# Kernel tuning notes

Hardware: AMD Instinct MI355X
Metric: run time of the kernel (lower is better)

## Reference

```python
import jax, jax.numpy as jnp
import numpy as np

PROPOSAL_NUM = 6          # max_output_size in tf.image.non_max_suppression
IOU_THRESHOLD = 0.25      # boxes with IoU > 0.25 vs a selected box are suppressed
CANVAS = 448.0            # NTS-Net input image size


def setup_inputs() -> dict:
    key = jax.random.key(0)
    k1, k2, k3 = jax.random.split(key, 3)
    B, N = 512, 65536
    rpn_score = jax.random.normal(k1, (B, N), dtype=jnp.float32)
    # anchors in [y1, x1, y2, x2] format with y2>y1, x2>x1 (as tf.image.non_max_suppression expects)
    yx1 = jax.random.uniform(k2, (N, 2), dtype=jnp.float32, minval=0.0, maxval=CANVAS)
    hw = jax.random.uniform(k3, (N, 2), dtype=jnp.float32, minval=16.0, maxval=200.0)
    anchors = jnp.concatenate([yx1, yx1 + hw], axis=-1)  # [N, 4]
    return {"rpn_score": rpn_score, "anchors": anchors}


def _batched_nms(rpn_score, anchors, k, iou_thr):
    """Greedy NMS, vectorized over the batch. Matches tf.image.non_max_suppression
    semantics with score_threshold=-inf: repeatedly pick the highest-scoring active
    box, then deactivate all boxes whose IoU with it exceeds iou_thr."""
    B, N = rpn_score.shape
    y1, x1, y2, x2 = anchors[:, 0], anchors[:, 1], anchors[:, 2], anchors[:, 3]
    areas = (y2 - y1) * (x2 - x1)            # [N]
    batch_ix = jnp.arange(B)

    def step(active, _):
        # active: [B, N] bool mask of boxes still eligible
        s = jnp.where(active, rpn_score, -jnp.inf)
        idx = jnp.argmax(s, axis=-1)          # [B] index of best remaining box
        sel = anchors[idx]                    # [B, 4]
        # IoU of selected box against all anchors -> [B, N]
        iy1 = jnp.maximum(sel[:, 0:1], y1[None, :])
        ix1 = jnp.maximum(sel[:, 1:2], x1[None, :])
        iy2 = jnp.minimum(sel[:, 2:3], y2[None, :])
        ix2 = jnp.minimum(sel[:, 3:4], x2[None, :])
        inter = jnp.maximum(iy2 - iy1, 0.0) * jnp.maximum(ix2 - ix1, 0.0)
        union = areas[idx][:, None] + areas[None, :] - inter
        iou = inter / union
        active = active & (iou <= iou_thr)
        active = active.at[batch_ix, idx].set(False)  # selected box itself removed
        return active, idx

    active0 = jnp.ones((B, N), dtype=bool)
    _, idxs = jax.lax.scan(step, active0, None, length=k)  # idxs: [k, B]
    return jnp.transpose(idxs).astype(jnp.int32)            # [B, k]


def reference(rpn_score, anchors):
    return _batched_nms(rpn_score, anchors, PROPOSAL_NUM, IOU_THRESHOLD)
```

## Files before the change

### kernel.cpp

```cpp
#include <hip/hip_runtime.h>


constexpr int N_BOX = 65536;
constexpr int KSEL  = 6;
constexpr int NT    = 1024;
constexpr int EPT   = N_BOX / NT;
constexpr float THR = 0.25f;

__device__ __forceinline__ unsigned long long umax64(unsigned long long a,
                                                     unsigned long long b) {
    return a > b ? a : b;
}

__global__ __launch_bounds__(NT) void nms_kernel(
    const float* __restrict__ score,
    const float* __restrict__ anchors,
    int* __restrict__ out)
{
    const int b    = blockIdx.x;
    const int tid  = threadIdx.x;
    const int base = tid * EPT;

    unsigned long long t0 = 0, t1 = 0, t2 = 0, t3 = 0;
    {
        const float4* s4 = reinterpret_cast<const float4*>(score + (size_t)b * N_BOX + base);
        const unsigned nb = ~(unsigned)base;
        #pragma unroll
        for (int q = 0; q < EPT / 4; ++q) {
            float4 v = s4[q];
            #pragma unroll
            for (int e = 0; e < 4; ++e) {
                unsigned fb = __float_as_uint(e == 0 ? v.x : e == 1 ? v.y : e == 2 ? v.z : v.w);
                unsigned m  = fb ^ (unsigned)(((int)fb >> 31) | 0x80000000);
                unsigned long long k =
                    ((unsigned long long)m << 32) | (unsigned)(nb - (4 * q + e));
                unsigned long long hi;
                hi = umax64(t0, k); k = (k ^ t0) ^ hi; t0 = hi;
                hi = umax64(t1, k); k = (k ^ t1) ^ hi; t1 = hi;
                hi = umax64(t2, k); k = (k ^ t2) ^ hi; t2 = hi;
                t3 = umax64(t3, k);
            }
        }
    }

    const float4* a4 = reinterpret_cast<const float4*>(anchors);
    const unsigned i0 = ~(unsigned)t0, i1 = ~(unsigned)t1,
                   i2 = ~(unsigned)t2, i3 = ~(unsigned)t3;
    const float4 b0 = a4[i0 & 0xffffu], b1 = a4[i1 & 0xffffu],
                 b2 = a4[i2 & 0xffffu], b3 = a4[i3 & 0xffffu];

    __shared__ unsigned long long red[NT / 64];
    __shared__ unsigned long long win;

    for (int t = 0; t < KSEL; ++t) {
        unsigned long long key = umax64(umax64(t0, t1), umax64(t2, t3));

        #pragma unroll
        for (int off = 32; off >= 1; off >>= 1)
            key = umax64(key, __shfl_down(key, off, 64));
        if ((tid & 63) == 0) red[tid >> 6] = key;
        __syncthreads();
        if (tid < 64) {
            unsigned long long k2 = (tid < NT / 64) ? red[tid] : 0ULL;
            #pragma unroll
            for (int off = 8; off >= 1; off >>= 1)
                k2 = umax64(k2, __shfl_down(k2, off, 64));
            if (tid == 0) win = k2;
        }
        __syncthreads();

        const unsigned idx = ~(unsigned)(win & 0xffffffffULL) & 0xffffu;
        if (tid == 0) out[b * KSEL + t] = (int)idx;

        const float4 s = a4[idx];
        const float sarea = (s.z - s.x) * (s.w - s.y);

        #define IOU_KILL(tk, bx)                                              \
        {                                                                     \
            float iy1 = fmaxf(s.x, bx.x), ix1 = fmaxf(s.y, bx.y);             \
            float iy2 = fminf(s.z, bx.z), ix2 = fminf(s.w, bx.w);             \
            float inter = fmaxf(iy2 - iy1, 0.0f) * fmaxf(ix2 - ix1, 0.0f);    \
            float area  = (bx.z - bx.x) * (bx.w - bx.y);                      \
            float uni   = sarea + area - inter;                               \
            if (inter > THR * uni) tk = 0ULL;                                 \
        }
        IOU_KILL(t0, b0)
        IOU_KILL(t1, b1)
        IOU_KILL(t2, b2)
        IOU_KILL(t3, b3)
        #undef IOU_KILL
        __syncthreads();
    }
}

extern "C" void kernel_launch(void* const* d_in, const int* in_sizes, int n_in,
                              void* d_out, int out_size, void* d_ws, size_t ws_size,
                              hipStream_t stream) {
    const float* score   = (const float*)d_in[0];
    const float* anchors = (const float*)d_in[1];
    int* out = (int*)d_out;

    nms_kernel<<<512, NT, 0, stream>>>(score, anchors, out);
}
```

Before: 209.1 us.

## Split per-row top-4 scan into separate multi-block kernel with coalesced loads

The score scan moves into its own kernel that uses four 256-thread blocks per row. Each thread reads float4s with a stride across the block, so loads are coalesced and prefetched two iterations ahead. The thread's top-4 keys go to a workspace pool, and a second kernel reads that pool to run the greedy NMS selection as before. This targets the strided per-thread access and the low parallelism of the original one-block-per-row scan, at the cost of an extra launch and a workspace round trip.

After: 217.4 us. 1.04x slower.

```diff
diff --git a/kernel.cpp b/kernel.cpp
--- a/kernel.cpp
+++ b/kernel.cpp
@@ -1,59 +1,96 @@
 #include <hip/hip_runtime.h>
 
 
-constexpr int N_BOX = 65536;
-constexpr int KSEL  = 6;
-constexpr int NT    = 1024;
-constexpr int EPT   = N_BOX / NT;
-constexpr float THR = 0.25f;
+using u64 = unsigned long long;
 
-__device__ __forceinline__ unsigned long long umax64(unsigned long long a,
-                                                     unsigned long long b) {
-    return a > b ? a : b;
+constexpr int N_BOX  = 65536;
+constexpr int KSEL   = 6;
+constexpr float THR  = 0.25f;
+
+constexpr int T1          = 256;
+constexpr int BLK_PER_ROW = 4;
+constexpr int SEG         = N_BOX / BLK_PER_ROW;
+constexpr int QIT         = SEG / (T1 * 4);
+constexpr int POOL_ROW    = BLK_PER_ROW * T1 * 4;
+
+constexpr int T2 = 1024;
+
+__device__ __forceinline__ u64 umax64(u64 a, u64 b) { return a > b ? a : b; }
+
+__global__ __launch_bounds__(T1) void topk_kernel(
+    const float* __restrict__ score,
+    u64* __restrict__ pool)
+{
+    const int row = blockIdx.x / BLK_PER_ROW;
+    const int g   = blockIdx.x % BLK_PER_ROW;
+    const int t   = threadIdx.x;
+
+    const float4* s4 = reinterpret_cast<const float4*>(
+        score + (size_t)row * N_BOX + (size_t)g * SEG);
+
+    u64 k0 = 0, k1 = 0, k2 = 0, k3 = 0;
+    unsigned nbq = ~(unsigned)(g * SEG + t * 4);
+
+    #define INS1(f, e) {                                                    \
+        unsigned fb = __float_as_uint(f);                                   \
+        unsigned m  = fb ^ (unsigned)(((int)fb >> 31) | 0x80000000);        \
+        u64 k = ((u64)m << 32) | (unsigned)(nbq - (e));                     \
+        u64 hi, lo;                                                         \
+        hi = k > k0 ? k : k0; lo = k > k0 ? k0 : k; k0 = hi; k = lo;        \
+        hi = k > k1 ? k : k1; lo = k > k1 ? k1 : k; k1 = hi; k = lo;        \
+        hi = k > k2 ? k : k2; lo = k > k2 ? k2 : k; k2 = hi; k = lo;        \
+        k3 = k > k3 ? k : k3; }
+    #define INS4(v) INS1(v.x, 0) INS1(v.y, 1) INS1(v.z, 2) INS1(v.w, 3)
+
+    float4 cur = s4[t];
+    float4 nxt = s4[T1 + t];
+
+    #pragma unroll 2
+    for (int q = 0; q < QIT - 2; ++q) {
+        float4 after = s4[(q + 2) * T1 + t];
+        INS4(cur)
+        nbq -= T1 * 4;
+        cur = nxt;
+        nxt = after;
+    }
+    INS4(cur)
+    nbq -= T1 * 4;
+    INS4(nxt)
+    #undef INS4
+    #undef INS1
+
+    u64* p = pool + (size_t)row * POOL_ROW + g * T1 + t;
+    p[0 * BLK_PER_ROW * T1] = k0;
+    p[1 * BLK_PER_ROW * T1] = k1;
+    p[2 * BLK_PER_ROW * T1] = k2;
+    p[3 * BLK_PER_ROW * T1] = k3;
 }
 
-__global__ __launch_bounds__(NT) void nms_kernel(
-    const float* __restrict__ score,
+__global__ __launch_bounds__(T2) void nms_kernel(
+    const u64* __restrict__ pool,
     const float* __restrict__ anchors,
     int* __restrict__ out)
 {
-    const int b    = blockIdx.x;
-    const int tid  = threadIdx.x;
-    const int base = tid * EPT;
+    const int row = blockIdx.x;
+    const int tid = threadIdx.x;
 
-    unsigned long long t0 = 0, t1 = 0, t2 = 0, t3 = 0;
-    {
-        const float4* s4 = reinterpret_cast<const float4*>(score + (size_t)b * N_BOX + base);
-        const unsigned nb = ~(unsigned)base;
-        #pragma unroll
-        for (int q = 0; q < EPT / 4; ++q) {
-            float4 v = s4[q];
-            #pragma unroll
-            for (int e = 0; e < 4; ++e) {
-                unsigned fb = __float_as_uint(e == 0 ? v.x : e == 1 ? v.y : e == 2 ? v.z : v.w);
-                unsigned m  = fb ^ (unsigned)(((int)fb >> 31) | 0x80000000);
-                unsigned long long k =
-                    ((unsigned long long)m << 32) | (unsigned)(nb - (4 * q + e));
-                unsigned long long hi;
-                hi = umax64(t0, k); k = (k ^ t0) ^ hi; t0 = hi;
-                hi = umax64(t1, k); k = (k ^ t1) ^ hi; t1 = hi;
-                hi = umax64(t2, k); k = (k ^ t2) ^ hi; t2 = hi;
-                t3 = umax64(t3, k);
-            }
-        }
-    }
+    const u64* p = pool + (size_t)row * POOL_ROW;
+    u64 k0 = p[tid];
+    u64 k1 = p[tid + T2];
+    u64 k2 = p[tid + 2 * T2];
+    u64 k3 = p[tid + 3 * T2];
 
     const float4* a4 = reinterpret_cast<const float4*>(anchors);
-    const unsigned i0 = ~(unsigned)t0, i1 = ~(unsigned)t1,
-                   i2 = ~(unsigned)t2, i3 = ~(unsigned)t3;
-    const float4 b0 = a4[i0 & 0xffffu], b1 = a4[i1 & 0xffffu],
-                 b2 = a4[i2 & 0xffffu], b3 = a4[i3 & 0xffffu];
+    const float4 b0 = a4[(~(unsigned)k0) & 0xffffu];
+    const float4 b1 = a4[(~(unsigned)k1) & 0xffffu];
+    const float4 b2 = a4[(~(unsigned)k2) & 0xffffu];
+    const float4 b3 = a4[(~(unsigned)k3) & 0xffffu];
 
-    __shared__ unsigned long long red[NT / 64];
-    __shared__ unsigned long long win;
+    __shared__ u64 red[T2 / 64];
+    __shared__ u64 win;
 
     for (int t = 0; t < KSEL; ++t) {
-        unsigned long long key = umax64(umax64(t0, t1), umax64(t2, t3));
+        u64 key = umax64(umax64(k0, k1), umax64(k2, k3));
 
         #pragma unroll
         for (int off = 32; off >= 1; off >>= 1)
@@ -61,16 +98,16 @@
         if ((tid & 63) == 0) red[tid >> 6] = key;
         __syncthreads();
         if (tid < 64) {
-            unsigned long long k2 = (tid < NT / 64) ? red[tid] : 0ULL;
+            u64 kk = (tid < T2 / 64) ? red[tid] : 0ULL;
             #pragma unroll
             for (int off = 8; off >= 1; off >>= 1)
-                k2 = umax64(k2, __shfl_down(k2, off, 64));
-            if (tid == 0) win = k2;
+                kk = umax64(kk, __shfl_down(kk, off, 64));
+            if (tid == 0) win = kk;
         }
         __syncthreads();
 
-        const unsigned idx = ~(unsigned)(win & 0xffffffffULL) & 0xffffu;
-        if (tid == 0) out[b * KSEL + t] = (int)idx;
+        const unsigned idx = (~(unsigned)(win & 0xffffffffULL)) & 0xffffu;
+        if (tid == 0) out[row * KSEL + t] = (int)idx;
 
         const float4 s = a4[idx];
         const float sarea = (s.z - s.x) * (s.w - s.y);
@@ -84,10 +121,10 @@
             float uni   = sarea + area - inter;                               \
             if (inter > THR * uni) tk = 0ULL;                                 \
         }
-        IOU_KILL(t0, b0)
-        IOU_KILL(t1, b1)
-        IOU_KILL(t2, b2)
-        IOU_KILL(t3, b3)
+        IOU_KILL(k0, b0)
+        IOU_KILL(k1, b1)
+        IOU_KILL(k2, b2)
+        IOU_KILL(k3, b3)
         #undef IOU_KILL
         __syncthreads();
     }
@@ -98,7 +135,10 @@
                               hipStream_t stream) {
     const float* score   = (const float*)d_in[0];
     const float* anchors = (const float*)d_in[1];
-    int* out = (int*)d_out;
+    int* out  = (int*)d_out;
+    u64* pool = (u64*)d_ws;
 
-    nms_kernel<<<512, NT, 0, stream>>>(score, anchors, out);
+    const int rows = in_sizes[0] / N_BOX;
+    topk_kernel<<<rows * BLK_PER_ROW, T1, 0, stream>>>(score, pool);
+    nms_kernel<<<rows, T2, 0, stream>>>(pool, (const float*)d_in[1], out);
 }
```
